# Kernel optimization log

Hardware: AMD Instinct MI355X
Metric: run time of the kernel (lower is better)

## Reference

```python
import jax, jax.numpy as jnp
import numpy as np

B, N_PER, SEQ, DIN, OUT = 16384, 16, 168, 16, 24
H1, H2, OUTF, NH, OLEN, DEG = 128, 128, 64, 4, 128, 4
DH = OUTF // NH
N = B * N_PER
E = N * DEG


def setup_inputs() -> dict:
    key = jax.random.key(0)
    ks = jax.random.split(key, 24)
    rng = np.random.default_rng(0)
    # DEG out-edges per node, destinations confined to the node's own graph block
    src = np.repeat(np.arange(N, dtype=np.int64), DEG)
    dst = (src // N_PER) * N_PER + rng.integers(0, N_PER, size=E).astype(np.int64)
    edge_index = jnp.stack([jnp.asarray(src), jnp.asarray(dst)])
    batch = jnp.asarray(np.arange(N, dtype=np.int64) // N_PER)
    g = lambda i, shape: jax.random.normal(ks[i], shape, jnp.float32) * 0.05
    return dict(
        x=jax.random.normal(ks[0], (N, SEQ), jnp.float32),
        y=jax.random.normal(ks[1], (N, OUT), jnp.float32),
        edge_index=edge_index, batch=batch,
        w1l=g(2, (SEQ, H1)), w1r=g(3, (SEQ, H1)), b1=jnp.zeros((H1,), jnp.float32),
        w2l=g(4, (H1, H2)), w2r=g(5, (H1, H2)), b2=jnp.zeros((H2,), jnp.float32),
        w3l=g(6, (H2, OUTF)), w3r=g(7, (H2, OUTF)), b3=jnp.zeros((OUTF,), jnp.float32),
        tcn_w=g(8, (OUTF, OUTF, 2)), tcn_b=jnp.zeros((OUTF,), jnp.float32),
        wq=g(9, (OUTF, OUTF)), wk=g(10, (OUTF, OUTF)), wv=g(11, (OUTF, OUTF)), wo=g(12, (OUTF, OUTF)),
        wproj=g(13, (OUTF, OLEN)), bproj=jnp.zeros((OLEN,), jnp.float32),
        fc1_w=g(14, (DIN, OLEN, 64)), fc1_b=jnp.zeros((DIN, 64), jnp.float32),
        fc2_w=g(15, (DIN, 64, OUT)), fc2_b=jnp.zeros((DIN, OUT), jnp.float32),
    )


def _sage(h, src, dst, wl, wr, b):
    # PyG SAGEConv: lin_l(mean-aggregated neighbors) + lin_r(self)
    agg = jax.ops.segment_sum(h[src], dst, num_segments=N)
    cnt = jax.ops.segment_sum(jnp.ones((src.shape[0],), h.dtype), dst, num_segments=N)
    agg = agg / jnp.maximum(cnt, 1.0)[:, None]
    return agg @ wl + h @ wr + b


def _forward(x, y, src, dst, w1l, w1r, b1, w2l, w2r, b2, w3l, w3r, b3,
             tcn_w, tcn_b, wq, wk, wv, wo, wproj, bproj, fc1_w, fc1_b, fc2_w, fc2_b):
    h = jax.nn.relu(_sage(x, src, dst, w1l, w1r, b1))
    h = jax.nn.relu(_sage(h, src, dst, w2l, w2r, b2))
    h = _sage(h, src, dst, w3l, w3r, b3)              # [N, 64]
    # ragged->dense batch: batch ids are block-constant with equal counts,
    # so the per-element Python stacking in the original is exactly a reshape
    xb = h.reshape(B, N_PER, OUTF)
    yb = y.reshape(B, N_PER, OUT)
    xt = xb.transpose(0, 2, 1)                        # [B, 64, n]
    # SMTA: causal TCN (kernel 2, channels [64]) with residual, dropout inert
    xp = jnp.pad(xt, ((0, 0), (0, 0), (1, 0)))
    conv = jax.lax.conv_general_dilated(xp, tcn_w, (1,), 'VALID',
                                        dimension_numbers=('NCH', 'OIH', 'NCH'))
    t = jax.nn.relu(conv + tcn_b[None, :, None]) + xt  # [B, 64, n]
    # 4-head self-attention over the node axis
    s = t.transpose(0, 2, 1)                          # [B, n, 64]
    q = (s @ wq).reshape(B, N_PER, NH, DH)
    k = (s @ wk).reshape(B, N_PER, NH, DH)
    v = (s @ wv).reshape(B, N_PER, NH, DH)
    scale = 1.0 / float(np.sqrt(DH))
    att = jax.nn.softmax(jnp.einsum('bqhd,bkhd->bhqk', q, k) * scale, axis=-1)
    o = jnp.einsum('bhqk,bkhd->bqhd', att, v).reshape(B, N_PER, OUTF) @ wo
    feat = o.mean(axis=1) @ wproj + bproj             # [B, 128]
    # per-variable fc heads, vectorized over the DIN heads
    h1 = jax.nn.relu(jnp.einsum('bf,kfh->kbh', feat, fc1_w) + fc1_b[:, None, :])
    pred = jnp.einsum('kbh,kho->kbo', h1, fc2_w) + fc2_b[:, None, :]  # [DIN, B, OUT]
    return pred, yb


def reference(x, y, edge_index, batch, w1l, w1r, b1, w2l, w2r, b2, w3l, w3r, b3,
              tcn_w, tcn_b, wq, wk, wv, wo, wproj, bproj, fc1_w, fc1_b, fc2_w, fc2_b):
    src, dst = edge_index[0], edge_index[1]
    return _forward(x, y, src, dst, w1l, w1r, b1, w2l, w2r, b2, w3l, w3r, b3,
                    tcn_w, tcn_b, wq, wk, wv, wo, wproj, bproj,
                    fc1_w, fc1_b, fc2_w, fc2_b)
```

## Files before the change

### kernel.cpp

```cpp
#include <hip/hip_runtime.h>
#include <cstdint>
#include <cstddef>


typedef __attribute__((ext_vector_type(8))) __bf16 bf16x8;
typedef __attribute__((ext_vector_type(4))) float  f32x4;

#define MFMA16(a,b,c) __builtin_amdgcn_mfma_f32_16x16x32_bf16((a),(b),(c),0,0,0)
#define FENCE() __threadfence_block()

#define NGR    16384
#define EDGES  1048576
#define PRED_ELEMS (16*16384*24)

#define O_W1L 0
#define O_W1R 24576
#define O_W2L 49152
#define O_W2R 65536
#define O_W3L 81920
#define O_W3R 90112
#define O_T0  98304
#define O_T1  102400
#define O_WQ  106496
#define O_WK  110592
#define O_WV  114688
#define O_WO  118784
#define O_FC1 122880
#define O_FC2 253952
#define O_FEAT 286720
#define PREP_TOT 286720

static __device__ __forceinline__ unsigned short f2bf(float f){
  unsigned int u = __builtin_bit_cast(unsigned int, f);
  u += 0x7FFFu + ((u >> 16) & 1u);
  return (unsigned short)(u >> 16);
}
static __device__ __forceinline__ float bf2f(unsigned short h){
  return __builtin_bit_cast(float, (unsigned int)h << 16);
}
static __device__ __forceinline__ bf16x8 ld8(const unsigned short* p){
  return __builtin_bit_cast(bf16x8, *(const uint4*)p);
}
static __device__ __forceinline__ bf16x8 zero8(){
  uint4 u = make_uint4(0u,0u,0u,0u);
  return __builtin_bit_cast(bf16x8, u);
}
static __device__ __forceinline__ unsigned int pkbf2(float a, float b){
  return (unsigned int)f2bf(a) | ((unsigned int)f2bf(b)<<16);
}
static __device__ __forceinline__ bf16x8 u4bf(unsigned int a, unsigned int b,
                                              unsigned int c, unsigned int d){
  uint4 u = make_uint4(a,b,c,d);
  return __builtin_bit_cast(bf16x8, u);
}
static __device__ __forceinline__ bf16x8 shfrag(unsigned int p0, unsigned int p1,
                                                int laneA, int laneB){
  return u4bf((unsigned int)__shfl((int)p0, laneA, 64),
              (unsigned int)__shfl((int)p1, laneA, 64),
              (unsigned int)__shfl((int)p0, laneB, 64),
              (unsigned int)__shfl((int)p1, laneB, 64));
}
static __device__ __forceinline__ bf16x8 xfrag(const float* __restrict__ xrow, int k0){
  int ks = (k0 < 168) ? k0 : 0;
  float4 f0 = *(const float4*)(xrow + ks);
  float4 f1 = *(const float4*)(xrow + ks + 4);
  return u4bf(pkbf2(f0.x,f0.y), pkbf2(f0.z,f0.w),
              pkbf2(f1.x,f1.y), pkbf2(f1.z,f1.w));
}
template<int TOT>
static __device__ __forceinline__ void sload(const unsigned short* __restrict__ src,
                                             int tid, uint4* r){
  #pragma unroll
  for (int i=0;i<TOT/2048;++i)
    r[i] = *(const uint4*)(src + i*2048 + tid*8);
  if constexpr ((TOT & 2047) != 0){
    if (tid < (TOT & 2047)/8)
      r[TOT/2048] = *(const uint4*)(src + (TOT/2048)*2048 + tid*8);
  }
}
template<int TOT,int K,int P>
static __device__ __forceinline__ void sstore(unsigned short* __restrict__ dst,
                                              int tid, const uint4* r){
  #pragma unroll
  for (int i=0;i<TOT/2048;++i){
    int idx = i*2048 + tid*8, row = idx / K;
    *(uint4*)(dst + row*P + (idx - row*K)) = r[i];
  }
  if constexpr ((TOT & 2047) != 0){
    if (tid < (TOT & 2047)/8){
      int idx = (TOT/2048)*2048 + tid*8, row = idx / K;
      *(uint4*)(dst + row*P + (idx - row*K)) = r[TOT/2048];
    }
  }
}
#define PH_NEXT(TOT,K,P) do{ sstore<TOT,K,P>(WB[cur^1], tid, rg); __syncthreads(); cur^=1; }while(0)

__global__ __launch_bounds__(256) void k_prep(
  const float* __restrict__ w1l, const float* __restrict__ w1r,
  const float* __restrict__ w2l, const float* __restrict__ w2r,
  const float* __restrict__ w3l, const float* __restrict__ w3r,
  const float* __restrict__ tcnw,
  const float* __restrict__ wq, const float* __restrict__ wk,
  const float* __restrict__ wv, const float* __restrict__ wo,
  const float* __restrict__ fc1w, const float* __restrict__ fc2w,
  unsigned short* __restrict__ W)
{
  int idx = blockIdx.x*256 + threadIdx.x;
  if (idx >= PREP_TOT) return;
  float v;
  if      (idx <  24576){ int t=idx;        int n=t/192,k=t%192; v=(k<168)? w1l[k*128+n]:0.f; }
  else if (idx <  49152){ int t=idx- 24576; int n=t/192,k=t%192; v=(k<168)? w1r[k*128+n]:0.f; }
  else if (idx <  65536){ int t=idx- 49152; int n=t/128,k=t%128; v=w2l[k*128+n]; }
  else if (idx <  81920){ int t=idx- 65536; int n=t/128,k=t%128; v=w2r[k*128+n]; }
  else if (idx <  90112){ int t=idx- 81920; int n=t/128,k=t%128; v=w3l[k*64+n]; }
  else if (idx <  98304){ int t=idx- 90112; int n=t/128,k=t%128; v=w3r[k*64+n]; }
  else if (idx < 102400){ int t=idx- 98304; int n=t/64, k=t%64;  v=tcnw[(n*64+k)*2+0]; }
  else if (idx < 106496){ int t=idx-102400; int n=t/64, k=t%64;  v=tcnw[(n*64+k)*2+1]; }
  else if (idx < 110592){ int t=idx-106496; int n=t/64, k=t%64;  v=wq[k*64+n]; }
  else if (idx < 114688){ int t=idx-110592; int n=t/64, k=t%64;  v=wk[k*64+n]; }
  else if (idx < 118784){ int t=idx-114688; int n=t/64, k=t%64;  v=wv[k*64+n]; }
  else if (idx < 122880){ int t=idx-118784; int n=t/64, k=t%64;  v=wo[k*64+n]; }
  else if (idx < 253952){ int t=idx-122880; int kh=t/8192, r=t%8192, n=r/128, k=r%128;
                          v=fc1w[kh*8192 + k*64 + n]; }
  else                  { int t=idx-253952; int kh=t/2048, r=t%2048, n=r/64,  k=r%64;
                          v=(n<24)? fc2w[kh*1536 + k*24 + n] : 0.f; }
  W[idx] = f2bf(v);
}

__global__ __launch_bounds__(256,3) void k_fused(
  const float* __restrict__ x, const int* __restrict__ edst,
  const float* __restrict__ b1, const float* __restrict__ b2,
  const float* __restrict__ b3, const float* __restrict__ tcnb,
  const float* __restrict__ wo, const float* __restrict__ wproj,
  const float* __restrict__ bproj,
  const unsigned short* __restrict__ ws0, unsigned short* __restrict__ feat)
{
  __shared__ alignas(16) unsigned char pool[4*9216];
  __shared__ alignas(16) unsigned short WB[2][4352];
  const int tid=threadIdx.x, w=tid>>6, lane=tid&63, quad=lane>>4, l15=lane&15;
  unsigned short* AR = (unsigned short*)(pool + w*9216);
  const int gb0 = (blockIdx.x*4 + w)*2;

  unsigned short* Hb = AR;
  unsigned short* X  = AR;
  unsigned short* T  = AR + 2304;
  unsigned short* Qb = AR;
  unsigned short* Pb = AR + 2304;
  float* OMf = (float*)AR;

  const bf16x8 Z = zero8();
  const f32x4  z = {0.f,0.f,0.f,0.f};
  const int laneA = 32*quad + l15, laneB = laneA + 16;

  uint4 rg[2];
  sload<3072>(ws0 + O_W1L, tid, rg);

  bf16x8 aA[2];
  #pragma unroll
  for (int g=0; g<2; ++g){
    int dl = edst[(gb0+g)*64 + lane] & 15;
    float c4[4]; float csum = 0.f;
    #pragma unroll
    for (int ss=0; ss<4; ++ss){
      int s = quad*4 + ss; int cc = 0;
      #pragma unroll
      for (int k=0;k<4;++k) cc += (__shfl(dl, s*4+k, 64) == l15) ? 1 : 0;
      c4[ss] = (float)cc; csum += (float)cc;
    }
    csum += __shfl_xor(csum, 16, 64);
    csum += __shfl_xor(csum, 32, 64);
    float ainv = 1.f / fmaxf(csum, 1.f);
    bf16x8 t = shfrag(pkbf2(c4[0]*ainv, c4[1]*ainv),
                      pkbf2(c4[2]*ainv, c4[3]*ainv), laneA, laneB);
    aA[g] = (quad < 2) ? t : Z;
  }

  const float* xr0 = x + (size_t)(gb0*16 + l15)*168;
  const float* xr1 = xr0 + 16*168;
  bf16x8 xa0[6], xa1[6];
  #pragma unroll
  for (int kc=0;kc<6;++kc){
    xa0[kc] = xfrag(xr0, kc*32 + quad*8);
    xa1[kc] = xfrag(xr1, kc*32 + quad*8);
  }

  int cur = 0;
  sstore<3072,192,200>(WB[0], tid, rg);
  __syncthreads();

  #pragma unroll
  for (int cg=0; cg<8; ++cg){
    sload<3072>(ws0 + O_W1R + cg*3072, tid, rg);
    f32x4 au0=z, au1_=z;
    #pragma unroll
    for (int kc=0;kc<6;++kc){
      bf16x8 bl = ld8(WB[cur] + l15*200 + kc*32 + quad*8);
      au0  = MFMA16(xa0[kc], bl, au0);
      au1_ = MFMA16(xa1[kc], bl, au1_);
    }
    bf16x8 uf0  = shfrag(pkbf2(au0[0],au0[1]),  pkbf2(au0[2],au0[3]),  laneA, laneB);
    bf16x8 uf1_ = shfrag(pkbf2(au1_[0],au1_[1]), pkbf2(au1_[2],au1_[3]), laneA, laneB);
    PH_NEXT(3072,192,200);

    if (cg < 7) sload<3072>(ws0 + O_W1L + (cg+1)*3072, tid, rg);
    else        sload<4096>(ws0 + O_W2L, tid, rg);
    f32x4 av0=z, av1_=z;
    #pragma unroll
    for (int kc=0;kc<6;++kc){
      bf16x8 br = ld8(WB[cur] + l15*200 + kc*32 + quad*8);
      av0  = MFMA16(xa0[kc], br, av0);
      av1_ = MFMA16(xa1[kc], br, av1_);
    }
    av0  = MFMA16(aA[0], uf0,  av0);
    av1_ = MFMA16(aA[1], uf1_, av1_);
    {
      float bb = b1[cg*16 + l15];
      #pragma unroll
      for (int r=0;r<4;++r){
        Hb[       (quad*4+r)*136 + cg*16 + l15] = f2bf(fmaxf(av0[r]+bb, 0.f));
        Hb[2176 + (quad*4+r)*136 + cg*16 + l15] = f2bf(fmaxf(av1_[r]+bb, 0.f));
      }
    }
    if (cg < 7){ PH_NEXT(3072,192,200); }
    else       { PH_NEXT(4096,128,136); }
  }
  FENCE();

  {
    ushort4 os[4][2][2];
    #pragma unroll
    for (int cg=0; cg<4; ++cg){
      sload<4096>(ws0 + O_W2R + cg*4096, tid, rg);
      bf16x8 uf[2][2];
      {
        f32x4 au[2][2] = {{z,z},{z,z}};
        #pragma unroll
        for (int kc=0;kc<4;++kc){
          bf16x8 a0 = ld8(Hb +        l15*136 + kc*32 + quad*8);
          bf16x8 a1 = ld8(Hb + 2176 + l15*136 + kc*32 + quad*8);
          #pragma unroll
          for (int c=0;c<2;++c){
            bf16x8 bl = ld8(WB[cur] + (c*16+l15)*136 + kc*32 + quad*8);
            au[0][c] = MFMA16(a0, bl, au[0][c]);
            au[1][c] = MFMA16(a1, bl, au[1][c]);
          }
        }
        #pragma unroll
        for (int g=0;g<2;++g)
        #pragma unroll
        for (int c=0;c<2;++c)
          uf[g][c] = shfrag(pkbf2(au[g][c][0],au[g][c][1]),
                            pkbf2(au[g][c][2],au[g][c][3]), laneA, laneB);
      }
      PH_NEXT(4096,128,136);

      if (cg < 3) sload<4096>(ws0 + O_W2L + (cg+1)*4096, tid, rg);
      else        sload<4096>(ws0 + O_W3L, tid, rg);
      {
        f32x4 av[2][2] = {{z,z},{z,z}};
        #pragma unroll
        for (int kc=0;kc<4;++kc){
          bf16x8 a0 = ld8(Hb +        l15*136 + kc*32 + quad*8);
          bf16x8 a1 = ld8(Hb + 2176 + l15*136 + kc*32 + quad*8);
          #pragma unroll
          for (int c=0;c<2;++c){
            bf16x8 br = ld8(WB[cur] + (c*16+l15)*136 + kc*32 + quad*8);
            av[0][c] = MFMA16(a0, br, av[0][c]);
            av[1][c] = MFMA16(a1, br, av[1][c]);
          }
        }
        #pragma unroll
        for (int g=0;g<2;++g)
        #pragma unroll
        for (int c=0;c<2;++c)
          av[g][c] = MFMA16(aA[g], uf[g][c], av[g][c]);
        #pragma unroll
        for (int c=0;c<2;++c){
          float bb = b2[cg*32 + c*16 + l15];
          #pragma unroll
          for (int g=0;g<2;++g){
            ushort4 p;
            p.x = f2bf(fmaxf(av[g][c][0]+bb, 0.f));
            p.y = f2bf(fmaxf(av[g][c][1]+bb, 0.f));
            p.z = f2bf(fmaxf(av[g][c][2]+bb, 0.f));
            p.w = f2bf(fmaxf(av[g][c][3]+bb, 0.f));
            os[cg][g][c] = p;
          }
        }
      }
      if (cg == 3){
        #pragma unroll
        for (int c2=0;c2<4;++c2)
        #pragma unroll
        for (int g=0;g<2;++g)
        #pragma unroll
        for (int c=0;c<2;++c){
          unsigned short* bp = Hb + g*2176 + c2*32 + c*16 + l15;
          ushort4 p = os[c2][g][c];
          bp[(quad*4+0)*136] = p.x;
          bp[(quad*4+1)*136] = p.y;
          bp[(quad*4+2)*136] = p.z;
          bp[(quad*4+3)*136] = p.w;
        }
        FENCE();
      }
      PH_NEXT(4096,128,136);
    }
  }

  bf16x8 uf3[2][4];
  f32x4  av3[2][4];
  {
    sload<4096>(ws0 + O_W3L + 4096, tid, rg);
    f32x4 au[2][2] = {{z,z},{z,z}};
    #pragma unroll
    for (int kc=0;kc<4;++kc){
      bf16x8 a0 = ld8(Hb +        l15*136 + kc*32 + quad*8);
      bf16x8 a1 = ld8(Hb + 2176 + l15*136 + kc*32 + quad*8);
      #pragma unroll
      for (int c=0;c<2;++c){
        bf16x8 bl = ld8(WB[cur] + (c*16+l15)*136 + kc*32 + quad*8);
        au[0][c] = MFMA16(a0, bl, au[0][c]);
        au[1][c] = MFMA16(a1, bl, au[1][c]);
      }
    }
    #pragma unroll
    for (int g=0;g<2;++g)
    #pragma unroll
    for (int c=0;c<2;++c)
      uf3[g][c] = shfrag(pkbf2(au[g][c][0],au[g][c][1]),
                         pkbf2(au[g][c][2],au[g][c][3]), laneA, laneB);
    PH_NEXT(4096,128,136);
  }
  {
    sload<4096>(ws0 + O_W3R, tid, rg);
    f32x4 au[2][2] = {{z,z},{z,z}};
    #pragma unroll
    for (int kc=0;kc<4;++kc){
      bf16x8 a0 = ld8(Hb +        l15*136 + kc*32 + quad*8);
      bf16x8 a1 = ld8(Hb + 2176 + l15*136 + kc*32 + quad*8);
      #pragma unroll
      for (int c=0;c<2;++c){
        bf16x8 bl = ld8(WB[cur] + (c*16+l15)*136 + kc*32 + quad*8);
        au[0][c] = MFMA16(a0, bl, au[0][c]);
        au[1][c] = MFMA16(a1, bl, au[1][c]);
      }
    }
    #pragma unroll
    for (int g=0;g<2;++g)
    #pragma unroll
    for (int c=0;c<2;++c)
      uf3[g][2+c] = shfrag(pkbf2(au[g][c][0],au[g][c][1]),
                           pkbf2(au[g][c][2],au[g][c][3]), laneA, laneB);
    PH_NEXT(4096,128,136);
  }
  {
    sload<4096>(ws0 + O_W3R + 4096, tid, rg);
    #pragma unroll
    for (int g=0;g<2;++g){ av3[g][0]=z; av3[g][1]=z; }
    #pragma unroll
    for (int kc=0;kc<4;++kc){
      bf16x8 a0 = ld8(Hb +        l15*136 + kc*32 + quad*8);
      bf16x8 a1 = ld8(Hb + 2176 + l15*136 + kc*32 + quad*8);
      #pragma unroll
      for (int c=0;c<2;++c){
        bf16x8 br = ld8(WB[cur] + (c*16+l15)*136 + kc*32 + quad*8);
        av3[0][c] = MFMA16(a0, br, av3[0][c]);
        av3[1][c] = MFMA16(a1, br, av3[1][c]);
      }
    }
    #pragma unroll
    for (int g=0;g<2;++g)
    #pragma unroll
    for (int c=0;c<2;++c)
      av3[g][c] = MFMA16(aA[g], uf3[g][c], av3[g][c]);
    PH_NEXT(4096,128,136);
  }
  {
    sload<2048>(ws0 + O_T0, tid, rg);
    #pragma unroll
    for (int g=0;g<2;++g){ av3[g][2]=z; av3[g][3]=z; }
    #pragma unroll
    for (int kc=0;kc<4;++kc){
      bf16x8 a0 = ld8(Hb +        l15*136 + kc*32 + quad*8);
      bf16x8 a1 = ld8(Hb + 2176 + l15*136 + kc*32 + quad*8);
      #pragma unroll
      for (int c=0;c<2;++c){
        bf16x8 br = ld8(WB[cur] + (c*16+l15)*136 + kc*32 + quad*8);
        av3[0][2+c] = MFMA16(a0, br, av3[0][2+c]);
        av3[1][2+c] = MFMA16(a1, br, av3[1][2+c]);
      }
    }
    #pragma unroll
    for (int g=0;g<2;++g)
    #pragma unroll
    for (int c=0;c<2;++c)
      av3[g][2+c] = MFMA16(aA[g], uf3[g][2+c], av3[g][2+c]);
    #pragma unroll
    for (int c=0;c<4;++c){
      float bb = b3[c*16 + l15];
      #pragma unroll
      for (int g=0;g<2;++g)
      #pragma unroll
      for (int r=0;r<4;++r)
        X[g*1152 + (quad*4+r)*72 + c*16 + l15] = f2bf(av3[g][c][r] + bb);
    }
    FENCE();
    PH_NEXT(2048,64,72);
  }

  {
    f32x4 acct[2][2] = {{z,z},{z,z}};
    {
      sload<2048>(ws0 + O_T1, tid, rg);
      #pragma unroll
      for (int kc=0;kc<2;++kc){
        bf16x8 as0 = (l15>0) ? ld8(X +        (l15-1)*72 + kc*32 + quad*8) : Z;
        bf16x8 as1 = (l15>0) ? ld8(X + 1152 + (l15-1)*72 + kc*32 + quad*8) : Z;
        #pragma unroll
        for (int c=0;c<2;++c){
          bf16x8 w0 = ld8(WB[cur] + (c*16+l15)*72 + kc*32 + quad*8);
          acct[0][c] = MFMA16(as0, w0, acct[0][c]);
          acct[1][c] = MFMA16(as1, w0, acct[1][c]);
        }
      }
      PH_NEXT(2048,64,72);
    }
    {
      sload<2048>(ws0 + O_T0 + 2048, tid, rg);
      #pragma unroll
      for (int kc=0;kc<2;++kc){
        bf16x8 ax0 = ld8(X +        l15*72 + kc*32 + quad*8);
        bf16x8 ax1 = ld8(X + 1152 + l15*72 + kc*32 + quad*8);
        #pragma unroll
        for (int c=0;c<2;++c){
          bf16x8 w1 = ld8(WB[cur] + (c*16+l15)*72 + kc*32 + quad*8);
          acct[0][c] = MFMA16(ax0, w1, acct[0][c]);
          acct[1][c] = MFMA16(ax1, w1, acct[1][c]);
        }
      }
      #pragma unroll
      for (int c=0;c<2;++c){
        int col = c*16 + l15;
        float tb = tcnb[col];
        #pragma unroll
        for (int g=0;g<2;++g)
        #pragma unroll
        for (int r=0;r<4;++r){
          float xr = bf2f(X[g*1152 + (quad*4+r)*72 + col]);
          T[g*1152 + (quad*4+r)*72 + col] = f2bf(fmaxf(acct[g][c][r]+tb, 0.f) + xr);
        }
      }
      PH_NEXT(2048,64,72);
    }
    f32x4 acc2[2][2] = {{z,z},{z,z}};
    {
      sload<2048>(ws0 + O_T1 + 2048, tid, rg);
      #pragma unroll
      for (int kc=0;kc<2;++kc){
        bf16x8 as0 = (l15>0) ? ld8(X +        (l15-1)*72 + kc*32 + quad*8) : Z;
        bf16x8 as1 = (l15>0) ? ld8(X + 1152 + (l15-1)*72 + kc*32 + quad*8) : Z;
        #pragma unroll
        for (int c=0;c<2;++c){
          bf16x8 w0 = ld8(WB[cur] + (c*16+l15)*72 + kc*32 + quad*8);
          acc2[0][c] = MFMA16(as0, w0, acc2[0][c]);
          acc2[1][c] = MFMA16(as1, w0, acc2[1][c]);
        }
      }
      PH_NEXT(2048,64,72);
    }
    {
      sload<2048>(ws0 + O_WQ, tid, rg);
      #pragma unroll
      for (int kc=0;kc<2;++kc){
        bf16x8 ax0 = ld8(X +        l15*72 + kc*32 + quad*8);
        bf16x8 ax1 = ld8(X + 1152 + l15*72 + kc*32 + quad*8);
        #pragma unroll
        for (int c=0;c<2;++c){
          bf16x8 w1 = ld8(WB[cur] + (c*16+l15)*72 + kc*32 + quad*8);
          acc2[0][c] = MFMA16(ax0, w1, acc2[0][c]);
          acc2[1][c] = MFMA16(ax1, w1, acc2[1][c]);
        }
      }
      #pragma unroll
      for (int c=0;c<2;++c){
        int col = 32 + c*16 + l15;
        float tb = tcnb[col];
        #pragma unroll
        for (int g=0;g<2;++g)
        #pragma unroll
        for (int r=0;r<4;++r){
          float xr = bf2f(X[g*1152 + (quad*4+r)*72 + col]);
          T[g*1152 + (quad*4+r)*72 + col] = f2bf(fmaxf(acc2[g][c][r]+tb, 0.f) + xr);
        }
      }
      FENCE();
      PH_NEXT(2048,64,72);
    }
  }

  {
    sload<2048>(ws0 + O_WQ + 2048, tid, rg);
    f32x4 aq[2][2] = {{z,z},{z,z}};
    #pragma unroll
    for (int kc=0;kc<2;++kc){
      bf16x8 t0 = ld8(T +        l15*72 + kc*32 + quad*8);
      bf16x8 t1 = ld8(T + 1152 + l15*72 + kc*32 + quad*8);
      #pragma unroll
      for (int c=0;c<2;++c){
        bf16x8 b = ld8(WB[cur] + (c*16+l15)*72 + kc*32 + quad*8);
        aq[0][c] = MFMA16(t0, b, aq[0][c]);
        aq[1][c] = MFMA16(t1, b, aq[1][c]);
      }
    }
    #pragma unroll
    for (int c=0;c<2;++c)
    #pragma unroll
    for (int g=0;g<2;++g)
    #pragma unroll
    for (int r=0;r<4;++r)
      Qb[g*1152 + (quad*4+r)*72 + c*16 + l15] = f2bf(aq[g][c][r]);
    PH_NEXT(2048,64,72);
  }
  {
    sload<2048>(ws0 + O_WK, tid, rg);
    f32x4 aq[2][2] = {{z,z},{z,z}};
    #pragma unroll
    for (int kc=0;kc<2;++kc){
      bf16x8 t0 = ld8(T +        l15*72 + kc*32 + quad*8);
      bf16x8 t1 = ld8(T + 1152 + l15*72 + kc*32 + quad*8);
      #pragma unroll
      for (int c=0;c<2;++c){
        bf16x8 b = ld8(WB[cur] + (c*16+l15)*72 + kc*32 + quad*8);
        aq[0][c] = MFMA16(t0, b, aq[0][c]);
        aq[1][c] = MFMA16(t1, b, aq[1][c]);
      }
    }
    #pragma unroll
    for (int c=0;c<2;++c)
    #pragma unroll
    for (int g=0;g<2;++g)
    #pragma unroll
    for (int r=0;r<4;++r)
      Qb[g*1152 + (quad*4+r)*72 + 32 + c*16 + l15] = f2bf(aq[g][c][r]);
    PH_NEXT(2048,64,72);
  }

  bf16x8 bK[2][4];
  {
    f32x4 kt[2][4];
    {
      sload<2048>(ws0 + O_WK + 2048, tid, rg);
      #pragma unroll
      for (int g=0;g<2;++g){ kt[g][0]=z; kt[g][1]=z; }
      #pragma unroll
      for (int kc=0;kc<2;++kc){
        bf16x8 t0 = ld8(T +        l15*72 + kc*32 + quad*8);
        bf16x8 t1 = ld8(T + 1152 + l15*72 + kc*32 + quad*8);
        #pragma unroll
        for (int c=0;c<2;++c){
          bf16x8 aW = ld8(WB[cur] + (c*16+l15)*72 + kc*32 + quad*8);
          kt[0][c] = MFMA16(aW, t0, kt[0][c]);
          kt[1][c] = MFMA16(aW, t1, kt[1][c]);
        }
      }
      PH_NEXT(2048,64,72);
    }
    {
      sload<2048>(ws0 + O_WV, tid, rg);
      #pragma unroll
      for (int g=0;g<2;++g){ kt[g][2]=z; kt[g][3]=z; }
      #pragma unroll
      for (int kc=0;kc<2;++kc){
        bf16x8 t0 = ld8(T +        l15*72 + kc*32 + quad*8);
        bf16x8 t1 = ld8(T + 1152 + l15*72 + kc*32 + quad*8);
        #pragma unroll
        for (int c=0;c<2;++c){
          bf16x8 aW = ld8(WB[cur] + (c*16+l15)*72 + kc*32 + quad*8);
          kt[0][2+c] = MFMA16(aW, t0, kt[0][2+c]);
          kt[1][2+c] = MFMA16(aW, t1, kt[1][2+c]);
        }
      }
      #pragma unroll
      for (int g=0;g<2;++g)
      #pragma unroll
      for (int c=0;c<4;++c){
        bf16x8 f = shfrag(pkbf2(kt[g][c][0],kt[g][c][1]),
                          pkbf2(kt[g][c][2],kt[g][c][3]), laneA, laneB);
        bK[g][c] = (quad < 2) ? f : Z;
      }
      PH_NEXT(2048,64,72);
    }
  }

  bf16x8 bV[2][4];
  {
    f32x4 vv[2][4];
    {
      sload<2048>(ws0 + O_WV + 2048, tid, rg);
      #pragma unroll
      for (int g=0;g<2;++g){ vv[g][0]=z; vv[g][1]=z; }
      #pragma unroll
      for (int kc=0;kc<2;++kc){
        bf16x8 t0 = ld8(T +        l15*72 + kc*32 + quad*8);
        bf16x8 t1 = ld8(T + 1152 + l15*72 + kc*32 + quad*8);
        #pragma unroll
        for (int c=0;c<2;++c){
          bf16x8 b = ld8(WB[cur] + (c*16+l15)*72 + kc*32 + quad*8);
          vv[0][c] = MFMA16(t0, b, vv[0][c]);
          vv[1][c] = MFMA16(t1, b, vv[1][c]);
        }
      }
      PH_NEXT(2048,64,72);
    }
    {
      #pragma unroll
      for (int g=0;g<2;++g){ vv[g][2]=z; vv[g][3]=z; }
      #pragma unroll
      for (int kc=0;kc<2;++kc){
        bf16x8 t0 = ld8(T +        l15*72 + kc*32 + quad*8);
        bf16x8 t1 = ld8(T + 1152 + l15*72 + kc*32 + quad*8);
        #pragma unroll
        for (int c=0;c<2;++c){
          bf16x8 b = ld8(WB[cur] + (c*16+l15)*72 + kc*32 + quad*8);
          vv[0][2+c] = MFMA16(t0, b, vv[0][2+c]);
          vv[1][2+c] = MFMA16(t1, b, vv[1][2+c]);
        }
      }
      #pragma unroll
      for (int g=0;g<2;++g)
      #pragma unroll
      for (int c=0;c<4;++c)
        bV[g][c] = shfrag(pkbf2(vv[g][c][0],vv[g][c][1]),
                          pkbf2(vv[g][c][2],vv[g][c][3]), laneA, laneB);
    }
  }
  FENCE();

  #pragma unroll
  for (int g=0; g<2; ++g){
    unsigned short* Pbg = Pb + g*1024;
    #pragma unroll
    for (int h=0;h<4;++h){
      bf16x8 aQ = (quad < 2) ? ld8(Qb + g*1152 + l15*72 + h*16 + quad*8) : Z;
      f32x4 s4 = MFMA16(aQ, bK[g][h], z);
      #pragma unroll
      for (int r=0;r<4;++r){
        float s = s4[r]*0.25f;
        float m = s;
        m = fmaxf(m, __shfl_xor(m,1,64));
        m = fmaxf(m, __shfl_xor(m,2,64));
        m = fmaxf(m, __shfl_xor(m,4,64));
        m = fmaxf(m, __shfl_xor(m,8,64));
        float p = __expf(s-m);
        float su = p;
        su += __shfl_xor(su,1,64);
        su += __shfl_xor(su,2,64);
        su += __shfl_xor(su,4,64);
        su += __shfl_xor(su,8,64);
        Pbg[(h*16 + quad*4 + r)*16 + l15] = f2bf(p/su);
      }
    }
  }
  FENCE();

  #pragma unroll
  for (int g=0; g<2; ++g){
    unsigned short* Pbg = Pb + g*1024;
    #pragma unroll
    for (int h=0;h<4;++h){
      bf16x8 aP = (quad < 2) ? ld8(Pbg + (h*16 + l15)*16 + quad*8) : Z;
      f32x4 o = MFMA16(aP, bV[g][h], z);
      float cs = o[0]+o[1]+o[2]+o[3];
      cs += __shfl_xor(cs, 16, 64);
      cs += __shfl_xor(cs, 32, 64);
      if (quad == 0) OMf[g*64 + h*16 + l15] = cs * (1.f/16.f);
    }
  }
  FENCE();

  {
    float t0 = 0.f, t1 = 0.f;
    #pragma unroll 8
    for (int d=0; d<64; ++d){
      float wv = wo[d*64 + lane];
      t0 += OMf[d]    * wv;
      t1 += OMf[64+d] * wv;
    }
    OMf[128+lane] = t0;
    OMf[192+lane] = t1;
    FENCE();
    float a00 = bproj[lane], a01 = bproj[lane+64];
    float a10 = a00, a11 = a01;
    #pragma unroll 8
    for (int m=0; m<64; ++m){
      float f0 = OMf[128+m], f1 = OMf[192+m];
      float w0 = wproj[m*128 + lane], w1 = wproj[m*128 + lane + 64];
      a00 += f0*w0; a01 += f0*w1;
      a10 += f1*w0; a11 += f1*w1;
    }
    feat[(size_t)gb0*128 + lane]        = f2bf(a00);
    feat[(size_t)gb0*128 + lane + 64]   = f2bf(a01);
    feat[(size_t)(gb0+1)*128 + lane]      = f2bf(a10);
    feat[(size_t)(gb0+1)*128 + lane + 64] = f2bf(a11);
  }
}

__global__ __launch_bounds__(256,4) void k_heads(
  const unsigned short* __restrict__ ws0,
  const float* __restrict__ fc1b, const float* __restrict__ fc2b,
  float* __restrict__ pred,
  const float4* __restrict__ ysrc, float4* __restrict__ ydst)
{
  __shared__ alignas(16) unsigned short W1s[64*136];
  __shared__ alignas(16) unsigned short W2s[32*72];
  __shared__ alignas(16) unsigned short hh[4*2304];
  const int tid=threadIdx.x, w=tid>>6, lane=tid&63, quad=lane>>4, l15=lane&15;
  const int kh = blockIdx.x >> 7;
  const int rb = (blockIdx.x & 127)*128 + w*32;
  unsigned short* hw = hh + w*2304;
  const unsigned short* featg = ws0 + O_FEAT;
  const unsigned short* W1 = ws0 + O_FC1 + kh*8192;
  const unsigned short* W2 = ws0 + O_FC2 + kh*2048;

  #pragma unroll
  for (int it=0; it<4; ++it){
    int idx = it*2048 + tid*8;
    int row = idx >> 7, col = idx & 127;
    *(uint4*)(W1s + row*136 + col) = *(const uint4*)(W1 + idx);
  }
  {
    int idx = tid*8; int row = idx >> 6, col = idx & 63;
    *(uint4*)(W2s + row*72 + col) = *(const uint4*)(W2 + idx);
  }
  __syncthreads();

  f32x4 z = {0.f,0.f,0.f,0.f};
  f32x4 acc[2][4];
  #pragma unroll
  for (int t=0;t<2;++t)
  #pragma unroll
  for (int c=0;c<4;++c) acc[t][c]=z;
  #pragma unroll
  for (int kc=0;kc<4;++kc){
    bf16x8 a0 = ld8(featg + (size_t)(rb+l15)*128    + kc*32+quad*8);
    bf16x8 a1 = ld8(featg + (size_t)(rb+16+l15)*128 + kc*32+quad*8);
    #pragma unroll
    for (int c=0;c<4;++c){
      bf16x8 b = ld8(W1s + (c*16+l15)*136 + kc*32+quad*8);
      acc[0][c] = MFMA16(a0, b, acc[0][c]);
      acc[1][c] = MFMA16(a1, b, acc[1][c]);
    }
  }
  #pragma unroll
  for (int c=0;c<4;++c){
    float bb = fc1b[kh*64 + c*16+l15];
    #pragma unroll
    for (int t=0;t<2;++t)
    #pragma unroll
    for (int r=0;r<4;++r)
      hw[t*1152 + (quad*4+r)*72 + c*16+l15] = f2bf(fmaxf(acc[t][c][r]+bb, 0.f));
  }
  FENCE();
  f32x4 acc2[2][2];
  #pragma unroll
  for (int t=0;t<2;++t)
  #pragma unroll
  for (int c=0;c<2;++c) acc2[t][c]=z;
  #pragma unroll
  for (int kc=0;kc<2;++kc){
    bf16x8 a0 = ld8(hw +        l15*72 + kc*32+quad*8);
    bf16x8 a1 = ld8(hw + 1152 + l15*72 + kc*32+quad*8);
    #pragma unroll
    for (int c=0;c<2;++c){
      bf16x8 b = ld8(W2s + (c*16+l15)*72 + kc*32+quad*8);
      acc2[0][c] = MFMA16(a0, b, acc2[0][c]);
      acc2[1][c] = MFMA16(a1, b, acc2[1][c]);
    }
  }
  FENCE();
  float* hf = (float*)hw;
  #pragma unroll
  for (int t=0;t<2;++t){
    #pragma unroll
    for (int c=0;c<2;++c){
      int col = c*16+l15;
      if (col < 24){
        float bb = fc2b[kh*24+col];
// ... 58 lines not shown
```

Before: 516.1 us.

## Stage weights via global_load_lds with XOR-swizzled layout and merge 64-wide phases

Replaces register-staged weight loads (global load into registers, then padded LDS store) with direct global-to-LDS async loads. Bank conflicts are avoided by an XOR swizzle baked into the prep-kernel layout instead of row padding. The TCN/Q/K/V stages now stage full 64x64 weight tiles per phase, which cuts the number of barriers and buffer swaps. This saves registers and VALU/LDS-store work, but relies on correct ordering of the async LDS writes with only __syncthreads between phases.

```diff
diff --git a/kernel.cpp b/kernel.cpp
--- a/kernel.cpp
+++ b/kernel.cpp
@@ -68,32 +68,23 @@
               pkbf2(f1.x,f1.y), pkbf2(f1.z,f1.w));
 }
 template<int TOT>
-static __device__ __forceinline__ void sload(const unsigned short* __restrict__ src,
-                                             int tid, uint4* r){
+static __device__ __forceinline__ void stageG(const unsigned short* __restrict__ src,
+                                              unsigned short* __restrict__ dst,
+                                              int w, int lane){
   #pragma unroll
   for (int i=0;i<TOT/2048;++i)
-    r[i] = *(const uint4*)(src + i*2048 + tid*8);
+    __builtin_amdgcn_global_load_lds(src + i*2048 + w*512 + lane*8,
+                                     dst + i*2048 + w*512, 16, 0, 0);
   if constexpr ((TOT & 2047) != 0){
-    if (tid < (TOT & 2047)/8)
-      r[TOT/2048] = *(const uint4*)(src + (TOT/2048)*2048 + tid*8);
-  }
-}
-template<int TOT,int K,int P>
-static __device__ __forceinline__ void sstore(unsigned short* __restrict__ dst,
-                                              int tid, const uint4* r){
-  #pragma unroll
-  for (int i=0;i<TOT/2048;++i){
-    int idx = i*2048 + tid*8, row = idx / K;
-    *(uint4*)(dst + row*P + (idx - row*K)) = r[i];
-  }
-  if constexpr ((TOT & 2047) != 0){
-    if (tid < (TOT & 2047)/8){
-      int idx = (TOT/2048)*2048 + tid*8, row = idx / K;
-      *(uint4*)(dst + row*P + (idx - row*K)) = r[TOT/2048];
-    }
-  }
-}
-#define PH_NEXT(TOT,K,P) do{ sstore<TOT,K,P>(WB[cur^1], tid, rg); __syncthreads(); cur^=1; }while(0)
+    if (w < (TOT & 2047)/512)
+      __builtin_amdgcn_global_load_lds(src + (TOT/2048)*2048 + w*512 + lane*8,
+                                       dst + (TOT/2048)*2048 + w*512, 16, 0, 0);
+  }
+}
+static __device__ __forceinline__ bf16x8 ldw(const unsigned short* slot, int K,
+                                             int row, int chunk){
+  return ld8(slot + row*K + (((chunk) ^ (row & 7)) << 3));
+}
 
 __global__ __launch_bounds__(256) void k_prep(
   const float* __restrict__ w1l, const float* __restrict__ w1r,
@@ -108,17 +99,30 @@
   int idx = blockIdx.x*256 + threadIdx.x;
   if (idx >= PREP_TOT) return;
   float v;
-  if      (idx <  24576){ int t=idx;        int n=t/192,k=t%192; v=(k<168)? w1l[k*128+n]:0.f; }
-  else if (idx <  49152){ int t=idx- 24576; int n=t/192,k=t%192; v=(k<168)? w1r[k*128+n]:0.f; }
-  else if (idx <  65536){ int t=idx- 49152; int n=t/128,k=t%128; v=w2l[k*128+n]; }
-  else if (idx <  81920){ int t=idx- 65536; int n=t/128,k=t%128; v=w2r[k*128+n]; }
-  else if (idx <  90112){ int t=idx- 81920; int n=t/128,k=t%128; v=w3l[k*64+n]; }
-  else if (idx <  98304){ int t=idx- 90112; int n=t/128,k=t%128; v=w3r[k*64+n]; }
-  else if (idx < 102400){ int t=idx- 98304; int n=t/64, k=t%64;  v=tcnw[(n*64+k)*2+0]; }
-  else if (idx < 106496){ int t=idx-102400; int n=t/64, k=t%64;  v=tcnw[(n*64+k)*2+1]; }
-  else if (idx < 110592){ int t=idx-106496; int n=t/64, k=t%64;  v=wq[k*64+n]; }
-  else if (idx < 114688){ int t=idx-110592; int n=t/64, k=t%64;  v=wk[k*64+n]; }
-  else if (idx < 118784){ int t=idx-114688; int n=t/64, k=t%64;  v=wv[k*64+n]; }
+  if      (idx <  24576){ int t=idx;        int n=t/192, ks=t%192;
+                          int k=(((ks>>3)^(n&7))<<3)+(ks&7);
+                          v=(k<168)? w1l[k*128+n]:0.f; }
+  else if (idx <  49152){ int t=idx- 24576; int n=t/192, ks=t%192;
+                          int k=(((ks>>3)^(n&7))<<3)+(ks&7);
+                          v=(k<168)? w1r[k*128+n]:0.f; }
+  else if (idx <  65536){ int t=idx- 49152; int n=t/128, ks=t%128;
+                          int k=(((ks>>3)^(n&7))<<3)+(ks&7); v=w2l[k*128+n]; }
+  else if (idx <  81920){ int t=idx- 65536; int n=t/128, ks=t%128;
+                          int k=(((ks>>3)^(n&7))<<3)+(ks&7); v=w2r[k*128+n]; }
+  else if (idx <  90112){ int t=idx- 81920; int n=t/128, ks=t%128;
+                          int k=(((ks>>3)^(n&7))<<3)+(ks&7); v=w3l[k*64+n]; }
+  else if (idx <  98304){ int t=idx- 90112; int n=t/128, ks=t%128;
+                          int k=(((ks>>3)^(n&7))<<3)+(ks&7); v=w3r[k*64+n]; }
+  else if (idx < 102400){ int t=idx- 98304; int n=t/64, ks=t%64;
+                          int k=(((ks>>3)^(n&7))<<3)+(ks&7); v=tcnw[(n*64+k)*2+0]; }
+  else if (idx < 106496){ int t=idx-102400; int n=t/64, ks=t%64;
+                          int k=(((ks>>3)^(n&7))<<3)+(ks&7); v=tcnw[(n*64+k)*2+1]; }
+  else if (idx < 110592){ int t=idx-106496; int n=t/64, ks=t%64;
+                          int k=(((ks>>3)^(n&7))<<3)+(ks&7); v=wq[k*64+n]; }
+  else if (idx < 114688){ int t=idx-110592; int n=t/64, ks=t%64;
+                          int k=(((ks>>3)^(n&7))<<3)+(ks&7); v=wk[k*64+n]; }
+  else if (idx < 118784){ int t=idx-114688; int n=t/64, ks=t%64;
+                          int k=(((ks>>3)^(n&7))<<3)+(ks&7); v=wv[k*64+n]; }
   else if (idx < 122880){ int t=idx-118784; int n=t/64, k=t%64;  v=wo[k*64+n]; }
   else if (idx < 253952){ int t=idx-122880; int kh=t/8192, r=t%8192, n=r/128, k=r%128;
                           v=fc1w[kh*8192 + k*64 + n]; }
@@ -136,7 +140,7 @@
   const unsigned short* __restrict__ ws0, unsigned short* __restrict__ feat)
 {
   __shared__ alignas(16) unsigned char pool[4*9216];
-  __shared__ alignas(16) unsigned short WB[2][4352];
+  __shared__ alignas(16) unsigned short WB[2][4096];
   const int tid=threadIdx.x, w=tid>>6, lane=tid&63, quad=lane>>4, l15=lane&15;
   unsigned short* AR = (unsigned short*)(pool + w*9216);
   const int gb0 = (blockIdx.x*4 + w)*2;
@@ -151,9 +155,10 @@
   const bf16x8 Z = zero8();
   const f32x4  z = {0.f,0.f,0.f,0.f};
   const int laneA = 32*quad + l15, laneB = laneA + 16;
-
-  uint4 rg[2];
-  sload<3072>(ws0 + O_W1L, tid, rg);
+  const int lx = l15 & 7;
+
+  int cur = 0;
+  stageG<3072>(ws0 + O_W1L, WB[0], w, lane);
 
   bf16x8 aA[2];
   #pragma unroll
@@ -183,31 +188,28 @@
     xa0[kc] = xfrag(xr0, kc*32 + quad*8);
     xa1[kc] = xfrag(xr1, kc*32 + quad*8);
   }
-
-  int cur = 0;
-  sstore<3072,192,200>(WB[0], tid, rg);
   __syncthreads();
 
   #pragma unroll
   for (int cg=0; cg<8; ++cg){
-    sload<3072>(ws0 + O_W1R + cg*3072, tid, rg);
+    stageG<3072>(ws0 + O_W1R + cg*3072, WB[cur^1], w, lane);
     f32x4 au0=z, au1_=z;
     #pragma unroll
     for (int kc=0;kc<6;++kc){
-      bf16x8 bl = ld8(WB[cur] + l15*200 + kc*32 + quad*8);
+      bf16x8 bl = ldw(WB[cur], 192, l15, kc*4+quad);
       au0  = MFMA16(xa0[kc], bl, au0);
       au1_ = MFMA16(xa1[kc], bl, au1_);
     }
-    bf16x8 uf0  = shfrag(pkbf2(au0[0],au0[1]),  pkbf2(au0[2],au0[3]),  laneA, laneB);
+    bf16x8 uf0  = shfrag(pkbf2(au0[0],au0[1]),   pkbf2(au0[2],au0[3]),   laneA, laneB);
     bf16x8 uf1_ = shfrag(pkbf2(au1_[0],au1_[1]), pkbf2(au1_[2],au1_[3]), laneA, laneB);
-    PH_NEXT(3072,192,200);
-
-    if (cg < 7) sload<3072>(ws0 + O_W1L + (cg+1)*3072, tid, rg);
-    else        sload<4096>(ws0 + O_W2L, tid, rg);
+    __syncthreads(); cur ^= 1;
+
+    if (cg < 7) stageG<3072>(ws0 + O_W1L + (cg+1)*3072, WB[cur^1], w, lane);
+    else        stageG<4096>(ws0 + O_W2L,               WB[cur^1], w, lane);
     f32x4 av0=z, av1_=z;
     #pragma unroll
     for (int kc=0;kc<6;++kc){
-      bf16x8 br = ld8(WB[cur] + l15*200 + kc*32 + quad*8);
+      bf16x8 br = ldw(WB[cur], 192, l15, kc*4+quad);
       av0  = MFMA16(xa0[kc], br, av0);
       av1_ = MFMA16(xa1[kc], br, av1_);
     }
@@ -221,8 +223,7 @@
         Hb[2176 + (quad*4+r)*136 + cg*16 + l15] = f2bf(fmaxf(av1_[r]+bb, 0.f));
       }
     }
-    if (cg < 7){ PH_NEXT(3072,192,200); }
-    else       { PH_NEXT(4096,128,136); }
+    __syncthreads(); cur ^= 1;
   }
   FENCE();
 
@@ -230,7 +231,7 @@
     ushort4 os[4][2][2];
     #pragma unroll
     for (int cg=0; cg<4; ++cg){
-      sload<4096>(ws0 + O_W2R + cg*4096, tid, rg);
+      stageG<4096>(ws0 + O_W2R + cg*4096, WB[cur^1], w, lane);
       bf16x8 uf[2][2];
       {
         f32x4 au[2][2] = {{z,z},{z,z}};
@@ -240,7 +241,7 @@
           bf16x8 a1 = ld8(Hb + 2176 + l15*136 + kc*32 + quad*8);
           #pragma unroll
           for (int c=0;c<2;++c){
-            bf16x8 bl = ld8(WB[cur] + (c*16+l15)*136 + kc*32 + quad*8);
+            bf16x8 bl = ldw(WB[cur], 128, c*16+l15, kc*4+quad);
             au[0][c] = MFMA16(a0, bl, au[0][c]);
             au[1][c] = MFMA16(a1, bl, au[1][c]);
           }
@@ -252,10 +253,10 @@
           uf[g][c] = shfrag(pkbf2(au[g][c][0],au[g][c][1]),
                             pkbf2(au[g][c][2],au[g][c][3]), laneA, laneB);
       }
-      PH_NEXT(4096,128,136);
-
-      if (cg < 3) sload<4096>(ws0 + O_W2L + (cg+1)*4096, tid, rg);
-      else        sload<4096>(ws0 + O_W3L, tid, rg);
+      __syncthreads(); cur ^= 1;
+
+      if (cg < 3) stageG<4096>(ws0 + O_W2L + (cg+1)*4096, WB[cur^1], w, lane);
+      else        stageG<4096>(ws0 + O_W3L,               WB[cur^1], w, lane);
       {
         f32x4 av[2][2] = {{z,z},{z,z}};
         #pragma unroll
@@ -264,7 +265,7 @@
           bf16x8 a1 = ld8(Hb + 2176 + l15*136 + kc*32 + quad*8);
           #pragma unroll
           for (int c=0;c<2;++c){
-            bf16x8 br = ld8(WB[cur] + (c*16+l15)*136 + kc*32 + quad*8);
+            bf16x8 br = ldw(WB[cur], 128, c*16+l15, kc*4+quad);
             av[0][c] = MFMA16(a0, br, av[0][c]);
             av[1][c] = MFMA16(a1, br, av[1][c]);
           }
@@ -304,14 +305,14 @@
         }
         FENCE();
       }
-      PH_NEXT(4096,128,136);
+      __syncthreads(); cur ^= 1;
     }
   }
 
   bf16x8 uf3[2][4];
   f32x4  av3[2][4];
   {
-    sload<4096>(ws0 + O_W3L + 4096, tid, rg);
+    stageG<4096>(ws0 + O_W3L + 4096, WB[cur^1], w, lane);
     f32x4 au[2][2] = {{z,z},{z,z}};
     #pragma unroll
     for (int kc=0;kc<4;++kc){
@@ -319,7 +320,7 @@
       bf16x8 a1 = ld8(Hb + 2176 + l15*136 + kc*32 + quad*8);
       #pragma unroll
       for (int c=0;c<2;++c){
-        bf16x8 bl = ld8(WB[cur] + (c*16+l15)*136 + kc*32 + quad*8);
+        bf16x8 bl = ldw(WB[cur], 128, c*16+l15, kc*4+quad);
         au[0][c] = MFMA16(a0, bl, au[0][c]);
         au[1][c] = MFMA16(a1, bl, au[1][c]);
       }
@@ -330,10 +331,10 @@
     for (int c=0;c<2;++c)
       uf3[g][c] = shfrag(pkbf2(au[g][c][0],au[g][c][1]),
                          pkbf2(au[g][c][2],au[g][c][3]), laneA, laneB);
-    PH_NEXT(4096,128,136);
-  }
-  {
-    sload<4096>(ws0 + O_W3R, tid, rg);
+    __syncthreads(); cur ^= 1;
+  }
+  {
+    stageG<4096>(ws0 + O_W3R, WB[cur^1], w, lane);
     f32x4 au[2][2] = {{z,z},{z,z}};
     #pragma unroll
     for (int kc=0;kc<4;++kc){
@@ -341,7 +342,7 @@
       bf16x8 a1 = ld8(Hb + 2176 + l15*136 + kc*32 + quad*8);
       #pragma unroll
       for (int c=0;c<2;++c){
-        bf16x8 bl = ld8(WB[cur] + (c*16+l15)*136 + kc*32 + quad*8);
+        bf16x8 bl = ldw(WB[cur], 128, c*16+l15, kc*4+quad);
         au[0][c] = MFMA16(a0, bl, au[0][c]);
         au[1][c] = MFMA16(a1, bl, au[1][c]);
       }
@@ -352,10 +353,10 @@
     for (int c=0;c<2;++c)
       uf3[g][2+c] = shfrag(pkbf2(au[g][c][0],au[g][c][1]),
                            pkbf2(au[g][c][2],au[g][c][3]), laneA, laneB);
-    PH_NEXT(4096,128,136);
-  }
-  {
-    sload<4096>(ws0 + O_W3R + 4096, tid, rg);
+    __syncthreads(); cur ^= 1;
+  }
+  {
+    stageG<4096>(ws0 + O_W3R + 4096, WB[cur^1], w, lane);
     #pragma unroll
     for (int g=0;g<2;++g){ av3[g][0]=z; av3[g][1]=z; }
     #pragma unroll
@@ -364,7 +365,7 @@
       bf16x8 a1 = ld8(Hb + 2176 + l15*136 + kc*32 + quad*8);
       #pragma unroll
       for (int c=0;c<2;++c){
-        bf16x8 br = ld8(WB[cur] + (c*16+l15)*136 + kc*32 + quad*8);
+        bf16x8 br = ldw(WB[cur], 128, c*16+l15, kc*4+quad);
         av3[0][c] = MFMA16(a0, br, av3[0][c]);
         av3[1][c] = MFMA16(a1, br, av3[1][c]);
       }
@@ -374,10 +375,10 @@
     #pragma unroll
     for (int c=0;c<2;++c)
       av3[g][c] = MFMA16(aA[g], uf3[g][c], av3[g][c]);
-    PH_NEXT(4096,128,136);
-  }
-  {
-    sload<2048>(ws0 + O_T0, tid, rg);
+    __syncthreads(); cur ^= 1;
+  }
+  {
+    stageG<4096>(ws0 + O_T0, WB[cur^1], w, lane);
     #pragma unroll
     for (int g=0;g<2;++g){ av3[g][2]=z; av3[g][3]=z; }
     #pragma unroll
@@ -386,7 +387,7 @@
       bf16x8 a1 = ld8(Hb + 2176 + l15*136 + kc*32 + quad*8);
       #pragma unroll
       for (int c=0;c<2;++c){
-        bf16x8 br = ld8(WB[cur] + (c*16+l15)*136 + kc*32 + quad*8);
+        bf16x8 br = ldw(WB[cur], 128, c*16+l15, kc*4+quad);
         av3[0][2+c] = MFMA16(a0, br, av3[0][2+c]);
         av3[1][2+c] = MFMA16(a1, br, av3[1][2+c]);
       }
@@ -406,234 +407,142 @@
         X[g*1152 + (quad*4+r)*72 + c*16 + l15] = f2bf(av3[g][c][r] + bb);
     }
     FENCE();
-    PH_NEXT(2048,64,72);
-  }
-
-  {
-    f32x4 acct[2][2] = {{z,z},{z,z}};
+    __syncthreads(); cur ^= 1;
+  }
+
+  {
+    f32x4 acct[2][4];
+    #pragma unroll
+    for (int g=0;g<2;++g)
+    #pragma unroll
+    for (int c=0;c<4;++c) acct[g][c]=z;
     {
-      sload<2048>(ws0 + O_T1, tid, rg);
+      stageG<4096>(ws0 + O_T1, WB[cur^1], w, lane);
       #pragma unroll
       for (int kc=0;kc<2;++kc){
         bf16x8 as0 = (l15>0) ? ld8(X +        (l15-1)*72 + kc*32 + quad*8) : Z;
         bf16x8 as1 = (l15>0) ? ld8(X + 1152 + (l15-1)*72 + kc*32 + quad*8) : Z;
         #pragma unroll
-        for (int c=0;c<2;++c){
-          bf16x8 w0 = ld8(WB[cur] + (c*16+l15)*72 + kc*32 + quad*8);
+        for (int c=0;c<4;++c){
+          bf16x8 w0 = ldw(WB[cur], 64, c*16+l15, kc*4+quad);
           acct[0][c] = MFMA16(as0, w0, acct[0][c]);
           acct[1][c] = MFMA16(as1, w0, acct[1][c]);
         }
       }
-      PH_NEXT(2048,64,72);
+      __syncthreads(); cur ^= 1;
     }
     {
-      sload<2048>(ws0 + O_T0 + 2048, tid, rg);
+      stageG<4096>(ws0 + O_WQ, WB[cur^1], w, lane);
       #pragma unroll
       for (int kc=0;kc<2;++kc){
         bf16x8 ax0 = ld8(X +        l15*72 + kc*32 + quad*8);
         bf16x8 ax1 = ld8(X + 1152 + l15*72 + kc*32 + quad*8);
         #pragma unroll
-        for (int c=0;c<2;++c){
-          bf16x8 w1 = ld8(WB[cur] + (c*16+l15)*72 + kc*32 + quad*8);
+        for (int c=0;c<4;++c){
+          bf16x8 w1 = ldw(WB[cur], 64, c*16+l15, kc*4+quad);
           acct[0][c] = MFMA16(ax0, w1, acct[0][c]);
           acct[1][c] = MFMA16(ax1, w1, acct[1][c]);
         }
       }
       #pragma unroll
-      for (int c=0;c<2;++c){
-        int col = c*16 + l15;
-        float tb = tcnb[col];
+      for (int c=0;c<4;++c){
+        float tb = tcnb[c*16 + l15];
         #pragma unroll
         for (int g=0;g<2;++g)
         #pragma unroll
         for (int r=0;r<4;++r){
-          float xr = bf2f(X[g*1152 + (quad*4+r)*72 + col]);
-          T[g*1152 + (quad*4+r)*72 + col] = f2bf(fmaxf(acct[g][c][r]+tb, 0.f) + xr);
+          float xr = bf2f(X[g*1152 + (quad*4+r)*72 + c*16 + l15]);
+          T[g*1152 + (quad*4+r)*72 + c*16 + l15] =
+              f2bf(fmaxf(acct[g][c][r]+tb, 0.f) + xr);
         }
       }
-      PH_NEXT(2048,64,72);
-    }
-    f32x4 acc2[2][2] = {{z,z},{z,z}};
-    {
-      sload<2048>(ws0 + O_T1 + 2048, tid, rg);
-      #pragma unroll
-      for (int kc=0;kc<2;++kc){
-        bf16x8 as0 = (l15>0) ? ld8(X +        (l15-1)*72 + kc*32 + quad*8) : Z;
-        bf16x8 as1 = (l15>0) ? ld8(X + 1152 + (l15-1)*72 + kc*32 + quad*8) : Z;
-        #pragma unroll
-        for (int c=0;c<2;++c){
-          bf16x8 w0 = ld8(WB[cur] + (c*16+l15)*72 + kc*32 + quad*8);
-          acc2[0][c] = MFMA16(as0, w0, acc2[0][c]);
-          acc2[1][c] = MFMA16(as1, w0, acc2[1][c]);
-        }
-      }
-      PH_NEXT(2048,64,72);
-    }
-    {
-      sload<2048>(ws0 + O_WQ, tid, rg);
-      #pragma unroll
-      for (int kc=0;kc<2;++kc){
-        bf16x8 ax0 = ld8(X +        l15*72 + kc*32 + quad*8);
-        bf16x8 ax1 = ld8(X + 1152 + l15*72 + kc*32 + quad*8);
-        #pragma unroll
-        for (int c=0;c<2;++c){
-          bf16x8 w1 = ld8(WB[cur] + (c*16+l15)*72 + kc*32 + quad*8);
-          acc2[0][c] = MFMA16(ax0, w1, acc2[0][c]);
-          acc2[1][c] = MFMA16(ax1, w1, acc2[1][c]);
-        }
-      }
-      #pragma unroll
-      for (int c=0;c<2;++c){
-        int col = 32 + c*16 + l15;
-        float tb = tcnb[col];
-        #pragma unroll
-        for (int g=0;g<2;++g)
-        #pragma unroll
-        for (int r=0;r<4;++r){
-          float xr = bf2f(X[g*1152 + (quad*4+r)*72 + col]);
-          T[g*1152 + (quad*4+r)*72 + col] = f2bf(fmaxf(acc2[g][c][r]+tb, 0.f) + xr);
-        }
-      }
       FENCE();
-      PH_NEXT(2048,64,72);
-    }
-  }
-
-  {
-    sload<2048>(ws0 + O_WQ + 2048, tid, rg);
-    f32x4 aq[2][2] = {{z,z},{z,z}};
+      __syncthreads(); cur ^= 1;
+    }
+  }
+
+  {
+    stageG<4096>(ws0 + O_WK, WB[cur^1], w, lane);
+    f32x4 aq[2][4];
+    #pragma unroll
+    for (int g=0;g<2;++g)
+    #pragma unroll
+    for (int c=0;c<4;++c) aq[g][c]=z;
     #pragma unroll
     for (int kc=0;kc<2;++kc){
       bf16x8 t0 = ld8(T +        l15*72 + kc*32 + quad*8);
       bf16x8 t1 = ld8(T + 1152 + l15*72 + kc*32 + quad*8);
       #pragma unroll
-      for (int c=0;c<2;++c){
-        bf16x8 b = ld8(WB[cur] + (c*16+l15)*72 + kc*32 + quad*8);
+      for (int c=0;c<4;++c){
+        bf16x8 b = ldw(WB[cur], 64, c*16+l15, kc*4+quad);
         aq[0][c] = MFMA16(t0, b, aq[0][c]);
         aq[1][c] = MFMA16(t1, b, aq[1][c]);
       }
     }
     #pragma unroll
-    for (int c=0;c<2;++c)
+    for (int c=0;c<4;++c)
     #pragma unroll
     for (int g=0;g<2;++g)
     #pragma unroll
     for (int r=0;r<4;++r)
       Qb[g*1152 + (quad*4+r)*72 + c*16 + l15] = f2bf(aq[g][c][r]);
-    PH_NEXT(2048,64,72);
-  }
-  {
-    sload<2048>(ws0 + O_WK, tid, rg);
-    f32x4 aq[2][2] = {{z,z},{z,z}};
+    __syncthreads(); cur ^= 1;
+  }
+
+  bf16x8 bK[2][4];
+  {
+    stageG<4096>(ws0 + O_WV, WB[cur^1], w, lane);
+    f32x4 kt[2][4];
+    #pragma unroll
+    for (int g=0;g<2;++g)
+    #pragma unroll
+    for (int c=0;c<4;++c) kt[g][c]=z;
     #pragma unroll
     for (int kc=0;kc<2;++kc){
       bf16x8 t0 = ld8(T +        l15*72 + kc*32 + quad*8);
       bf16x8 t1 = ld8(T + 1152 + l15*72 + kc*32 + quad*8);
       #pragma unroll
-      for (int c=0;c<2;++c){
-        bf16x8 b = ld8(WB[cur] + (c*16+l15)*72 + kc*32 + quad*8);
-        aq[0][c] = MFMA16(t0, b, aq[0][c]);
-        aq[1][c] = MFMA16(t1, b, aq[1][c]);
-      }
-    }
-    #pragma unroll
-    for (int c=0;c<2;++c)
-    #pragma unroll
-    for (int g=0;g<2;++g)
-    #pragma unroll
-    for (int r=0;r<4;++r)
-      Qb[g*1152 + (quad*4+r)*72 + 32 + c*16 + l15] = f2bf(aq[g][c][r]);
-    PH_NEXT(2048,64,72);
-  }
-
-  bf16x8 bK[2][4];
-  {
-    f32x4 kt[2][4];
-    {
-      sload<2048>(ws0 + O_WK + 2048, tid, rg);
-      #pragma unroll
-      for (int g=0;g<2;++g){ kt[g][0]=z; kt[g][1]=z; }
-      #pragma unroll
-      for (int kc=0;kc<2;++kc){
-        bf16x8 t0 = ld8(T +        l15*72 + kc*32 + quad*8);
-        bf16x8 t1 = ld8(T + 1152 + l15*72 + kc*32 + quad*8);
-        #pragma unroll
-        for (int c=0;c<2;++c){
-          bf16x8 aW = ld8(WB[cur] + (c*16+l15)*72 + kc*32 + quad*8);
-          kt[0][c] = MFMA16(aW, t0, kt[0][c]);
-          kt[1][c] = MFMA16(aW, t1, kt[1][c]);
-        }
-      }
-      PH_NEXT(2048,64,72);
-    }
-    {
-      sload<2048>(ws0 + O_WV, tid, rg);
-      #pragma unroll
-      for (int g=0;g<2;++g){ kt[g][2]=z; kt[g][3]=z; }
-      #pragma unroll
-      for (int kc=0;kc<2;++kc){
-        bf16x8 t0 = ld8(T +        l15*72 + kc*32 + quad*8);
-        bf16x8 t1 = ld8(T + 1152 + l15*72 + kc*32 + quad*8);
-        #pragma unroll
-        for (int c=0;c<2;++c){
-          bf16x8 aW = ld8(WB[cur] + (c*16+l15)*72 + kc*32 + quad*8);
-          kt[0][2+c] = MFMA16(aW, t0, kt[0][2+c]);
-          kt[1][2+c] = MFMA16(aW, t1, kt[1][2+c]);
-        }
-      }
-      #pragma unroll
-      for (int g=0;g<2;++g)
-      #pragma unroll
       for (int c=0;c<4;++c){
-        bf16x8 f = shfrag(pkbf2(kt[g][c][0],kt[g][c][1]),
-                          pkbf2(kt[g][c][2],kt[g][c][3]), laneA, laneB);
-        bK[g][c] = (quad < 2) ? f : Z;
-      }
-      PH_NEXT(2048,64,72);
-    }
+        bf16x8 aW = ldw(WB[cur], 64, c*16+l15, kc*4+quad);
+        kt[0][c] = MFMA16(aW, t0, kt[0][c]);
+        kt[1][c] = MFMA16(aW, t1, kt[1][c]);
+      }
+    }
+    #pragma unroll
+    for (int g=0;g<2;++g)
+    #pragma unroll
+    for (int c=0;c<4;++c){
+      bf16x8 f = shfrag(pkbf2(kt[g][c][0],kt[g][c][1]),
+                        pkbf2(kt[g][c][2],kt[g][c][3]), laneA, laneB);
+      bK[g][c] = (quad < 2) ? f : Z;
+    }
+    __syncthreads(); cur ^= 1;
   }
 
   bf16x8 bV[2][4];
   {
     f32x4 vv[2][4];
-    {
-      sload<2048>(ws0 + O_WV + 2048, tid, rg);
-      #pragma unroll
-      for (int g=0;g<2;++g){ vv[g][0]=z; vv[g][1]=z; }
-      #pragma unroll
-      for (int kc=0;kc<2;++kc){
-        bf16x8 t0 = ld8(T +        l15*72 + kc*32 + quad*8);
-        bf16x8 t1 = ld8(T + 1152 + l15*72 + kc*32 + quad*8);
-        #pragma unroll
-        for (int c=0;c<2;++c){
-          bf16x8 b = ld8(WB[cur] + (c*16+l15)*72 + kc*32 + quad*8);
-          vv[0][c] = MFMA16(t0, b, vv[0][c]);
-          vv[1][c] = MFMA16(t1, b, vv[1][c]);
-        }
-      }
-      PH_NEXT(2048,64,72);
-    }
-    {
-      #pragma unroll
-      for (int g=0;g<2;++g){ vv[g][2]=z; vv[g][3]=z; }
-      #pragma unroll
-      for (int kc=0;kc<2;++kc){
-        bf16x8 t0 = ld8(T +        l15*72 + kc*32 + quad*8);
-        bf16x8 t1 = ld8(T + 1152 + l15*72 + kc*32 + quad*8);
-        #pragma unroll
-        for (int c=0;c<2;++c){
-          bf16x8 b = ld8(WB[cur] + (c*16+l15)*72 + kc*32 + quad*8);
-          vv[0][2+c] = MFMA16(t0, b, vv[0][2+c]);
-          vv[1][2+c] = MFMA16(t1, b, vv[1][2+c]);
-        }
-      }
-      #pragma unroll
-      for (int g=0;g<2;++g)
-      #pragma unroll
-      for (int c=0;c<4;++c)
-        bV[g][c] = shfrag(pkbf2(vv[g][c][0],vv[g][c][1]),
-                          pkbf2(vv[g][c][2],vv[g][c][3]), laneA, laneB);
-    }
+    #pragma unroll
+    for (int g=0;g<2;++g)
+    #pragma unroll
+    for (int c=0;c<4;++c) vv[g][c]=z;
+    #pragma unroll
+    for (int kc=0;kc<2;++kc){
+      bf16x8 t0 = ld8(T +        l15*72 + kc*32 + quad*8);
+      bf16x8 t1 = ld8(T + 1152 + l15*72 + kc*32 + quad*8);
+      #pragma unroll
+      for (int c=0;c<4;++c){
+        bf16x8 b = ldw(WB[cur], 64, c*16+l15, kc*4+quad);
+        vv[0][c] = MFMA16(t0, b, vv[0][c]);
+        vv[1][c] = MFMA16(t1, b, vv[1][c]);
+      }
+    }
+    #pragma unroll
+    for (int g=0;g<2;++g)
+    #pragma unroll
+    for (int c=0;c<4;++c)
+      bV[g][c] = shfrag(pkbf2(vv[g][c][0],vv[g][c][1]),
+                        pkbf2(vv[g][c][2],vv[g][c][3]), laneA, laneB);
   }
   FENCE();
 
```

Result: faster. 458.5 us (-11.2%).
